# Kernel optimization log

Hardware: AMD Instinct MI355X
Metric: run time of the kernel (lower is better)

## Reference

```python
import jax, jax.numpy as jnp
import numpy as np

B, D, E, K, H = 16384, 1024, 6, 2, 256  # tokens, d_in, n_experts, top-k, expert hidden
EPS = 0.1  # epsilon default from forward signature


def setup_inputs() -> dict:
    key = jax.random.key(0)
    ks = jax.random.split(key, 4)
    scaled = lambda k, shp, fan: (jax.random.normal(k, shp, jnp.float32) / np.float32(np.sqrt(fan)))
    return {
        "x": jax.random.normal(ks[0], (B, D), jnp.float32),
        "Wr": scaled(ks[1], (D, E), D),
        "br": jnp.zeros((E,), jnp.float32),
        "W1": scaled(ks[2], (E, D, H), D),
        "b1": jnp.zeros((E, H), jnp.float32),
        "W2": scaled(ks[3], (E, H, D), H),
        "b2": jnp.zeros((E, D), jnp.float32),
    }


def reference(x, Wr, br, W1, b1, W2, b2):
    logits = x @ Wr + br                              # [B,E]
    probs = jax.nn.softmax(logits, axis=-1)
    En = probs.shape[-1]
    probs = (1.0 - EPS) * probs + EPS / En            # epsilon-annealed mix
    wts, idx = jax.lax.top_k(probs, K)                # [B,K] each, descending
    load = probs.mean(axis=0)                         # [E]
    aux = (load * jnp.log(load * En + 1e-9)).sum() / np.float32(np.log(En + 1e-9))
    # Dense all-expert evaluation (exact math of per-token expert MLPs), then gather top-k.
    h = jax.nn.gelu(jnp.einsum('bd,edh->ebh', x, W1) + b1[:, None, :], approximate=False)  # [E,B,H]
    ex_out = jnp.einsum('ebh,ehd->ebd', h, W2) + b2[:, None, :]                            # [E,B,D]
    tok = jnp.arange(x.shape[0])
    picked = ex_out[idx.T, tok[None, :]]              # [K,B,D] gather chosen experts
    out = jnp.einsum('bk,kbd->bd', wts, picked)       # weighted combine
    return out, aux
```

## Files before the change

### kernel.cpp

```cpp
#include <hip/hip_runtime.h>
#include <hip/hip_bf16.h>
#include <math.h>

#define B_TOK 16384
#define DDIM  1024
#define NEXP  6
#define NPAIR 15
#define HDIM  256
#define EPSF  0.1f
#define TILE  32
#define MAXTILES (B_TOK / TILE + NPAIR)

typedef float f32x4 __attribute__((ext_vector_type(4)));
typedef short bf16x8 __attribute__((ext_vector_type(8)));

__device__ __forceinline__ unsigned short f2bf(float f) {
    unsigned int u = __float_as_uint(f);
    u += 0x7FFFu + ((u >> 16) & 1u);
    return (unsigned short)(u >> 16);
}
__device__ __forceinline__ int pack2bf(float a, float b) {
    return (int)f2bf(a) | ((int)f2bf(b) << 16);
}
__device__ __forceinline__ float gelu_exact(float v) {
    return 0.5f * v * (1.0f + erff(v * 0.70710678118654752440f));
}

__global__ __launch_bounds__(256) void pack_w1_kernel(
    const float* __restrict__ W1, unsigned short* __restrict__ w1p) {
    const int lane = threadIdx.x & 63;
    const int blob = blockIdx.x * 4 + (threadIdx.x >> 6);
    const int e  = blob >> 9;
    const int rm = blob & 511;
    const int mg = rm >> 5;
    const int ks = rm & 31;
    const int d0 = ks * 32 + (lane >> 4) * 8;
    const int h  = mg * 16 + (lane & 15);
    const float* src = W1 + ((size_t)e * DDIM + d0) * HDIM + h;
    ushort4 o0, o1;
    o0.x = f2bf(src[0 * HDIM]); o0.y = f2bf(src[1 * HDIM]);
    o0.z = f2bf(src[2 * HDIM]); o0.w = f2bf(src[3 * HDIM]);
    o1.x = f2bf(src[4 * HDIM]); o1.y = f2bf(src[5 * HDIM]);
    o1.z = f2bf(src[6 * HDIM]); o1.w = f2bf(src[7 * HDIM]);
    unsigned short* dst = w1p + ((size_t)blob * 512) + lane * 8;
    *reinterpret_cast<ushort4*>(dst)     = o0;
    *reinterpret_cast<ushort4*>(dst + 4) = o1;
}

__global__ __launch_bounds__(256) void pack_w2_kernel(
    const float* __restrict__ W2, unsigned short* __restrict__ w2p) {
    const int lane = threadIdx.x & 63;
    const int blob = blockIdx.x * 4 + (threadIdx.x >> 6);
    const int e  = blob >> 9;
    const int rm = blob & 511;
    const int dg = rm >> 3;
    const int hs = rm & 7;
    const int h0 = hs * 32 + (lane >> 4) * 8;
    const int d  = dg * 16 + (lane & 15);
    const float* src = W2 + ((size_t)e * HDIM + h0) * DDIM + d;
    ushort4 o0, o1;
    o0.x = f2bf(src[0 * DDIM]); o0.y = f2bf(src[1 * DDIM]);
    o0.z = f2bf(src[2 * DDIM]); o0.w = f2bf(src[3 * DDIM]);
    o1.x = f2bf(src[4 * DDIM]); o1.y = f2bf(src[5 * DDIM]);
    o1.z = f2bf(src[6 * DDIM]); o1.w = f2bf(src[7 * DDIM]);
    unsigned short* dst = w2p + ((size_t)blob * 512) + lane * 8;
    *reinterpret_cast<ushort4*>(dst)     = o0;
    *reinterpret_cast<ushort4*>(dst + 4) = o1;
}

__global__ __launch_bounds__(256) void router1_kernel(
    const float* __restrict__ x, const float* __restrict__ Wr, const float* __restrict__ br,
    int* __restrict__ erec, float2* __restrict__ wrec, float* __restrict__ partial) {
    __shared__ float ls[NEXP];
    const int tid = threadIdx.x;
    if (tid < NEXP) ls[tid] = 0.0f;
    __syncthreads();

    const int wave = tid >> 6;
    const int lane = tid & 63;
    const int tok0 = blockIdx.x * 16 + wave * 4;

    float acc[4][NEXP];
#pragma unroll
    for (int j = 0; j < 4; ++j)
#pragma unroll
        for (int e = 0; e < NEXP; ++e) acc[j][e] = 0.0f;

#pragma unroll
    for (int it = 0; it < 4; ++it) {
        const float4* w4 = reinterpret_cast<const float4*>(
            Wr + (size_t)(it * 256 + lane * 4) * NEXP);
        float w[24];
#pragma unroll
        for (int q = 0; q < 6; ++q) *reinterpret_cast<float4*>(&w[q * 4]) = w4[q];
#pragma unroll
        for (int j = 0; j < 4; ++j) {
            float4 xv = reinterpret_cast<const float4*>(
                x + (size_t)(tok0 + j) * DDIM)[it * 64 + lane];
            float xa[4] = {xv.x, xv.y, xv.z, xv.w};
#pragma unroll
            for (int i2 = 0; i2 < 4; ++i2)
#pragma unroll
                for (int e = 0; e < NEXP; ++e)
                    acc[j][e] += xa[i2] * w[i2 * NEXP + e];
        }
    }

    float lsacc[NEXP];
#pragma unroll
    for (int e = 0; e < NEXP; ++e) lsacc[e] = 0.0f;

#pragma unroll
    for (int j = 0; j < 4; ++j) {
        float p[NEXP];
        float m = -1e30f;
#pragma unroll
        for (int e = 0; e < NEXP; ++e) {
            float v = acc[j][e];
#pragma unroll
            for (int off = 32; off > 0; off >>= 1) v += __shfl_xor(v, off, 64);
            p[e] = v + br[e];
            m = fmaxf(m, p[e]);
        }
        float s = 0.0f;
#pragma unroll
        for (int e = 0; e < NEXP; ++e) { p[e] = expf(p[e] - m); s += p[e]; }
        const float inv = (1.0f - EPSF) / s;
#pragma unroll
        for (int e = 0; e < NEXP; ++e) p[e] = p[e] * inv + EPSF / (float)NEXP;

        int b1i = 0; float bp = p[0];
#pragma unroll
        for (int e = 1; e < NEXP; ++e) if (p[e] > bp) { bp = p[e]; b1i = e; }
        int b2i = -1; float sp = -1e30f;
#pragma unroll
        for (int e = 0; e < NEXP; ++e) if (e != b1i && p[e] > sp) { sp = p[e]; b2i = e; }

        if (lane == 0) {
            erec[tok0 + j] = b1i | (b2i << 16);
            wrec[tok0 + j] = make_float2(bp, sp);
        }
#pragma unroll
        for (int e = 0; e < NEXP; ++e) lsacc[e] += p[e];
    }

    if (lane == 0) {
#pragma unroll
        for (int e = 0; e < NEXP; ++e) atomicAdd(&ls[e], lsacc[e]);
    }
    __syncthreads();
    if (tid < NEXP) partial[blockIdx.x * NEXP + tid] = ls[tid];
}

__global__ __launch_bounds__(1024) void router2_kernel(
    const int* __restrict__ erec, const float2* __restrict__ wrec,
    int* __restrict__ plist, float2* __restrict__ wpair, int* __restrict__ cnt) {
    __shared__ int lc[NPAIR];
    __shared__ int gb[NPAIR];
    const int tid = threadIdx.x;
    if (tid < NPAIR) lc[tid] = 0;
    __syncthreads();

    const int tok = blockIdx.x * 1024 + tid;
    const int er = erec[tok];
    const float2 wr = wrec[tok];
    const int e1 = er & 0xffff;
    const int e2 = er >> 16;
    const int a = min(e1, e2);
    const int b = max(e1, e2);
    const float wa = (a == e1) ? wr.x : wr.y;
    const float wb = (a == e1) ? wr.y : wr.x;
    const int p = a * (11 - a) / 2 + (b - a - 1);

    const int i = atomicAdd(&lc[p], 1);
    __syncthreads();
    if (tid < NPAIR) gb[tid] = atomicAdd(&cnt[tid], lc[tid]);
    __syncthreads();

    const int pos = gb[p] + i;
    plist[p * B_TOK + pos] = tok;
    wpair[p * B_TOK + pos] = make_float2(wa, wb);
}

__global__ void router3_aux_kernel(const int* __restrict__ cnt, int* __restrict__ table,
                                   const float* __restrict__ partial, float* __restrict__ out) {
    const int lane = threadIdx.x;
    if (lane == 0) {
        int off = 0;
        for (int p = 0; p < NPAIR; ++p) {
            const int t = (cnt[p] + TILE - 1) / TILE;
            for (int i = 0; i < t; ++i) table[1 + off + i] = (p << 16) | i;
            off += t;
        }
        table[0] = off;
    }
    float s[NEXP];
#pragma unroll
    for (int e = 0; e < NEXP; ++e) s[e] = 0.0f;
    for (int i = lane; i < 1024; i += 64) {
#pragma unroll
        for (int e = 0; e < NEXP; ++e) s[e] += partial[i * NEXP + e];
    }
#pragma unroll
    for (int e = 0; e < NEXP; ++e) {
        float v = s[e];
#pragma unroll
        for (int off = 32; off > 0; off >>= 1) v += __shfl_xor(v, off, 64);
        s[e] = v;
    }
    if (lane == 0) {
        float a = 0.0f;
#pragma unroll
        for (int e = 0; e < NEXP; ++e) {
            float ld = s[e] / (float)B_TOK;
            a += ld * logf(ld * (float)NEXP + 1e-9f);
        }
        out[(size_t)B_TOK * DDIM] = a / logf((float)NEXP + 1e-9f);
    }
}

__global__ __launch_bounds__(512, 2) void expert_kernel(
    const float* __restrict__ x,
    const unsigned short* __restrict__ w1p,
    const unsigned short* __restrict__ w2p,
    const float* __restrict__ b1,
    const float* __restrict__ b2,
    const int* __restrict__ plist, const float2* __restrict__ wpair,
    const int* __restrict__ cnt, const int* __restrict__ table,
    float* __restrict__ out) {
    const int g = blockIdx.x;
    if (g >= table[0]) return;
    const int code = table[1 + g];
    const int p = code >> 16;
    const int lt = code & 0xffff;
    const int n = cnt[p];

    int a, b;
    if      (p < 5)  { a = 0; b = p + 1; }
    else if (p < 9)  { a = 1; b = p - 3; }
    else if (p < 12) { a = 2; b = p - 6; }
    else if (p < 14) { a = 3; b = p - 8; }
    else             { a = 4; b = 5; }

    __shared__ int   tok_l[TILE];
    __shared__ float wa_l[TILE];
    __shared__ float wb_l[TILE];
    __shared__ __align__(16) char smem[65536];

    const int tid = threadIdx.x;
    const int lane = tid & 63;
    const int wave = tid >> 6;

    if (tid < TILE) {
        const int gi = lt * TILE + tid;
        if (gi < n) {
            tok_l[tid] = plist[p * B_TOK + gi];
            float2 w2v = wpair[p * B_TOK + gi];
            wa_l[tid] = w2v.x; wb_l[tid] = w2v.y;
        } else { tok_l[tid] = -1; wa_l[tid] = 0.0f; wb_l[tid] = 0.0f; }
    }
    __syncthreads();

    {
        const int ti = tid >> 4;
        const int q  = tid & 15;
        const int tok_s = tok_l[ti];
        const float* xrow = x + (size_t)(tok_s < 0 ? 0 : tok_s) * DDIM;
#pragma unroll
        for (int it = 0; it < 8; ++it) {
            const int k0 = it * 128 + q * 8;
            float4 f0, f1;
            if (tok_s >= 0) {
                const float4* ps = reinterpret_cast<const float4*>(xrow + k0);
                f0 = ps[0]; f1 = ps[1];
            } else {
                f0 = make_float4(0.f, 0.f, 0.f, 0.f); f1 = f0;
            }
            int4 wv;
            wv.x = pack2bf(f0.x, f0.y); wv.y = pack2bf(f0.z, f0.w);
            wv.z = pack2bf(f1.x, f1.y); wv.w = pack2bf(f1.z, f1.w);
            const int c = k0 >> 3;
            *reinterpret_cast<int4*>(smem + ti * 2048 + ((c ^ (ti & 7)) << 4)) = wv;
        }
    }
    __syncthreads();

    const int wexp = (wave < 4) ? a : b;
    const int hrow0 = (wave & 3) * 64;
    const int kofs = (lane >> 4) * 8;

    const unsigned short* w1base = w1p + ((size_t)wexp * 16 + (wave & 3) * 4) * 32 * 512
                                       + lane * 8;

    f32x4 zero4 = {0.f, 0.f, 0.f, 0.f};
    f32x4 acc[4][2];
#pragma unroll
    for (int i = 0; i < 4; ++i) { acc[i][0] = zero4; acc[i][1] = zero4; }

#pragma unroll 4
    for (int ks = 0; ks < 32; ++ks) {
        const int kk = ks * 32;
        bf16x8 aF[4], bF[2];
#pragma unroll
        for (int nt = 0; nt < 2; ++nt) {
            const int t = nt * 16 + (lane & 15);
            const int c = (kk >> 3) + (lane >> 4);
            bF[nt] = *reinterpret_cast<const bf16x8*>(
                smem + t * 2048 + ((c ^ (t & 7)) << 4));
        }
#pragma unroll
        for (int mt = 0; mt < 4; ++mt)
            aF[mt] = *reinterpret_cast<const bf16x8*>(
                w1base + ((size_t)mt * 32 + ks) * 512);
#pragma unroll
        for (int mt = 0; mt < 4; ++mt)
#pragma unroll
            for (int nt = 0; nt < 2; ++nt)
                acc[mt][nt] = __builtin_amdgcn_mfma_f32_16x16x32_bf16(
                    aF[mt], bF[nt], acc[mt][nt], 0, 0, 0);
    }
    __syncthreads();

    char* hdst = smem + ((wave < 4) ? 0 : 16384);
#pragma unroll
    for (int mt = 0; mt < 4; ++mt) {
        const int hh0 = hrow0 + mt * 16 + (lane >> 4) * 4;
        const float4 bb = *reinterpret_cast<const float4*>(b1 + wexp * HDIM + hh0);
#pragma unroll
        for (int nt = 0; nt < 2; ++nt) {
            const int t = nt * 16 + (lane & 15);
            const float wt = (wave < 4) ? wa_l[t] : wb_l[t];
            ushort4 hv;
            hv.x = f2bf(wt * gelu_exact(acc[mt][nt][0] + bb.x));
            hv.y = f2bf(wt * gelu_exact(acc[mt][nt][1] + bb.y));
            hv.z = f2bf(wt * gelu_exact(acc[mt][nt][2] + bb.z));
            hv.w = f2bf(wt * gelu_exact(acc[mt][nt][3] + bb.w));
            int off = t * 512 + hh0 * 2; off ^= (t & 7) << 4;
            *reinterpret_cast<ushort4*>(hdst + off) = hv;
        }
    }
    __syncthreads();

#pragma unroll 1
    for (int c2 = 0; c2 < 2; ++c2) {
        const int dbase = wave * 128 + c2 * 64;
        const unsigned short* w2abase = w2p + ((size_t)a * 64 + wave * 8 + c2 * 4) * 8 * 512
                                            + lane * 8;
        const unsigned short* w2bbase = w2p + ((size_t)b * 64 + wave * 8 + c2 * 4) * 8 * 512
                                            + lane * 8;
        f32x4 a2[2][4];
#pragma unroll
        for (int i = 0; i < 2; ++i)
#pragma unroll
            for (int j = 0; j < 4; ++j) a2[i][j] = zero4;

#pragma unroll
        for (int hs = 0; hs < 8; ++hs) {
            const int hh0 = hs * 32;
            bf16x8 aF[2], bF[4];
#pragma unroll
            for (int mt = 0; mt < 2; ++mt) {
                const int t = mt * 16 + (lane & 15);
                int off = t * 512 + (hh0 + kofs) * 2; off ^= (t & 7) << 4;
                aF[mt] = *reinterpret_cast<const bf16x8*>(smem + off);
            }
#pragma unroll
            for (int nt = 0; nt < 4; ++nt)
                bF[nt] = *reinterpret_cast<const bf16x8*>(
                    w2abase + ((size_t)nt * 8 + hs) * 512);
#pragma unroll
            for (int mt = 0; mt < 2; ++mt)
#pragma unroll
                for (int nt = 0; nt < 4; ++nt)
                    a2[mt][nt] = __builtin_amdgcn_mfma_f32_16x16x32_bf16(
                        aF[mt], bF[nt], a2[mt][nt], 0, 0, 0);
        }
#pragma unroll
        for (int hs = 0; hs < 8; ++hs) {
            const int hh0 = hs * 32;
            bf16x8 aF[2], bF[4];
#pragma unroll
            for (int mt = 0; mt < 2; ++mt) {
                const int t = mt * 16 + (lane & 15);
                int off = t * 512 + (hh0 + kofs) * 2; off ^= (t & 7) << 4;
                aF[mt] = *reinterpret_cast<const bf16x8*>(smem + 16384 + off);
            }
#pragma unroll
            for (int nt = 0; nt < 4; ++nt)
                bF[nt] = *reinterpret_cast<const bf16x8*>(
                    w2bbase + ((size_t)nt * 8 + hs) * 512);
#pragma unroll
            for (int mt = 0; mt < 2; ++mt)
#pragma unroll
                for (int nt = 0; nt < 4; ++nt)
                    a2[mt][nt] = __builtin_amdgcn_mfma_f32_16x16x32_bf16(
                        aF[mt], bF[nt], a2[mt][nt], 0, 0, 0);
        }

#pragma unroll
        for (int mt = 0; mt < 2; ++mt) {
            const int t0 = mt * 16 + (lane >> 4) * 4;
            int tkj[4]; float waj[4], wbj[4];
#pragma unroll
            for (int j = 0; j < 4; ++j) {
                tkj[j] = tok_l[t0 + j]; waj[j] = wa_l[t0 + j]; wbj[j] = wb_l[t0 + j];
            }
#pragma unroll
            for (int nt = 0; nt < 4; ++nt) {
                const int d = dbase + nt * 16 + (lane & 15);
                const float bA = b2[a * DDIM + d];
                const float bB = b2[b * DDIM + d];
#pragma unroll
                for (int j = 0; j < 4; ++j) {
                    if (tkj[j] >= 0)
                        out[(size_t)tkj[j] * DDIM + d] =
                            a2[mt][nt][j] + waj[j] * bA + wbj[j] * bB;
                }
            }
        }
    }
}

extern "C" void kernel_launch(void* const* d_in, const int* in_sizes, int n_in,
                              void* d_out, int out_size, void* d_ws, size_t ws_size,
                              hipStream_t stream) {
    const float* x  = (const float*)d_in[0];
    const float* Wr = (const float*)d_in[1];
    const float* br = (const float*)d_in[2];
    const float* W1 = (const float*)d_in[3];
    const float* b1 = (const float*)d_in[4];
    const float* W2 = (const float*)d_in[5];
    const float* b2 = (const float*)d_in[6];
    float* out = (float*)d_out;

    char* ws = (char*)d_ws;
    unsigned short* w1p   = (unsigned short*)(ws + 0);
    unsigned short* w2p   = (unsigned short*)(ws + 3145728);
    int*            plist = (int*)(ws + 6291456);
    float2*         wpair = (float2*)(ws + 7274496);
    int*            erec  = (int*)(ws + 9240576);
    float2*         wrec  = (float2*)(ws + 9306112);
    float*          partial = (float*)(ws + 9437184);
    int*            cnt   = (int*)(ws + 9461760);
    int*            table = (int*)(ws + 9462016);

    hipMemsetAsync(cnt, 0, 256, stream);

    pack_w1_kernel<<<dim3(768), dim3(256), 0, stream>>>(W1, w1p);
    pack_w2_kernel<<<dim3(768), dim3(256), 0, stream>>>(W2, w2p);

    router1_kernel<<<dim3(B_TOK / 16), dim3(256), 0, stream>>>(x, Wr, br, erec, wrec, partial);
    router2_kernel<<<dim3(B_TOK / 1024), dim3(1024), 0, stream>>>(erec, wrec, plist, wpair, cnt);
    router3_aux_kernel<<<1, 64, 0, stream>>>(cnt, table, partial, out);
    expert_kernel<<<dim3(MAXTILES), dim3(512), 0, stream>>>(
        x, w1p, w2p, b1, b2, plist, wpair, cnt, table, out);
}
```

Baseline: 302.3 us.

## Stream x tile through double-buffered LDS chunks to cut shared memory

The expert kernel no longer stages the full 32x1024 bf16 x tile in LDS before the first GEMM. It now loads x in eight 128-column chunks into a double buffer, prefetching the next chunk into registers while MFMAs run on the current one. This shrinks LDS use from 64KB to 48KB and raises launch bounds to 3 blocks per CU to improve occupancy. The cost is two extra barriers per chunk and more register pressure under the tighter occupancy bound.

```diff
diff --git a/kernel.cpp b/kernel.cpp
--- a/kernel.cpp
+++ b/kernel.cpp
@@ -219,7 +219,7 @@
     }
 }
 
-__global__ __launch_bounds__(512, 2) void expert_kernel(
+__global__ __launch_bounds__(512, 3) void expert_kernel(
     const float* __restrict__ x,
     const unsigned short* __restrict__ w1p,
     const unsigned short* __restrict__ w2p,
@@ -245,7 +245,7 @@
     __shared__ int   tok_l[TILE];
     __shared__ float wa_l[TILE];
     __shared__ float wb_l[TILE];
-    __shared__ __align__(16) char smem[65536];
+    __shared__ __align__(16) char smem[49152];
 
     const int tid = threadIdx.x;
     const int lane = tid & 63;
@@ -261,29 +261,11 @@
     }
     __syncthreads();
 
-    {
-        const int ti = tid >> 4;
-        const int q  = tid & 15;
-        const int tok_s = tok_l[ti];
-        const float* xrow = x + (size_t)(tok_s < 0 ? 0 : tok_s) * DDIM;
-#pragma unroll
-        for (int it = 0; it < 8; ++it) {
-            const int k0 = it * 128 + q * 8;
-            float4 f0, f1;
-            if (tok_s >= 0) {
-                const float4* ps = reinterpret_cast<const float4*>(xrow + k0);
-                f0 = ps[0]; f1 = ps[1];
-            } else {
-                f0 = make_float4(0.f, 0.f, 0.f, 0.f); f1 = f0;
-            }
-            int4 wv;
-            wv.x = pack2bf(f0.x, f0.y); wv.y = pack2bf(f0.z, f0.w);
-            wv.z = pack2bf(f1.x, f1.y); wv.w = pack2bf(f1.z, f1.w);
-            const int c = k0 >> 3;
-            *reinterpret_cast<int4*>(smem + ti * 2048 + ((c ^ (ti & 7)) << 4)) = wv;
-        }
-    }
-    __syncthreads();
+    const int ti = tid >> 4;
+    const int q  = tid & 15;
+    const int tok_s = tok_l[ti];
+    const float* xrow = x + (size_t)(tok_s < 0 ? 0 : tok_s) * DDIM;
+    const int woff = ti * 256 + ((q ^ (ti & 7)) << 4);
 
     const int wexp = (wave < 4) ? a : b;
     const int hrow0 = (wave & 3) * 64;
@@ -297,31 +279,59 @@
 #pragma unroll
     for (int i = 0; i < 4; ++i) { acc[i][0] = zero4; acc[i][1] = zero4; }
 
-#pragma unroll 4
-    for (int ks = 0; ks < 32; ++ks) {
-        const int kk = ks * 32;
-        bf16x8 aF[4], bF[2];
-#pragma unroll
-        for (int nt = 0; nt < 2; ++nt) {
-            const int t = nt * 16 + (lane & 15);
-            const int c = (kk >> 3) + (lane >> 4);
-            bF[nt] = *reinterpret_cast<const bf16x8*>(
-                smem + t * 2048 + ((c ^ (t & 7)) << 4));
-        }
-#pragma unroll
-        for (int mt = 0; mt < 4; ++mt)
-            aF[mt] = *reinterpret_cast<const bf16x8*>(
-                w1base + ((size_t)mt * 32 + ks) * 512);
-#pragma unroll
-        for (int mt = 0; mt < 4; ++mt)
-#pragma unroll
-            for (int nt = 0; nt < 2; ++nt)
-                acc[mt][nt] = __builtin_amdgcn_mfma_f32_16x16x32_bf16(
-                    aF[mt], bF[nt], acc[mt][nt], 0, 0, 0);
-    }
-    __syncthreads();
-
-    char* hdst = smem + ((wave < 4) ? 0 : 16384);
+    float4 pf0, pf1;
+    {
+        const float4* ps = reinterpret_cast<const float4*>(xrow + q * 8);
+        pf0 = ps[0]; pf1 = ps[1];
+        int4 wv;
+        wv.x = pack2bf(pf0.x, pf0.y); wv.y = pack2bf(pf0.z, pf0.w);
+        wv.z = pack2bf(pf1.x, pf1.y); wv.w = pack2bf(pf1.z, pf1.w);
+        if (tok_s < 0) wv = make_int4(0, 0, 0, 0);
+        *reinterpret_cast<int4*>(smem + woff) = wv;
+    }
+    __syncthreads();
+
+#pragma unroll 1
+    for (int c = 0; c < 8; ++c) {
+        char* cur = smem + ((c & 1) << 13);
+        char* nxt = smem + (((c + 1) & 1) << 13);
+        if (c < 7) {
+            const float4* ps = reinterpret_cast<const float4*>(xrow + (c + 1) * 128 + q * 8);
+            pf0 = ps[0]; pf1 = ps[1];
+        }
+#pragma unroll
+        for (int ks = 0; ks < 4; ++ks) {
+            bf16x8 aF[4], bF[2];
+#pragma unroll
+            for (int nt = 0; nt < 2; ++nt) {
+                const int t = nt * 16 + (lane & 15);
+                const int ci = ks * 4 + (lane >> 4);
+                bF[nt] = *reinterpret_cast<const bf16x8*>(
+                    cur + t * 256 + ((ci ^ (t & 7)) << 4));
+            }
+#pragma unroll
+            for (int mt = 0; mt < 4; ++mt)
+                aF[mt] = *reinterpret_cast<const bf16x8*>(
+                    w1base + ((size_t)mt * 32 + c * 4 + ks) * 512);
+#pragma unroll
+            for (int mt = 0; mt < 4; ++mt)
+#pragma unroll
+                for (int nt = 0; nt < 2; ++nt)
+                    acc[mt][nt] = __builtin_amdgcn_mfma_f32_16x16x32_bf16(
+                        aF[mt], bF[nt], acc[mt][nt], 0, 0, 0);
+        }
+        __syncthreads();
+        if (c < 7) {
+            int4 wv;
+            wv.x = pack2bf(pf0.x, pf0.y); wv.y = pack2bf(pf0.z, pf0.w);
+            wv.z = pack2bf(pf1.x, pf1.y); wv.w = pack2bf(pf1.z, pf1.w);
+            if (tok_s < 0) wv = make_int4(0, 0, 0, 0);
+            *reinterpret_cast<int4*>(nxt + woff) = wv;
+            __syncthreads();
+        }
+    }
+
+    char* hdst = smem + ((wave < 4) ? 16384 : 32768);
 #pragma unroll
     for (int mt = 0; mt < 4; ++mt) {
         const int hh0 = hrow0 + mt * 16 + (lane >> 4) * 4;
@@ -362,7 +372,7 @@
             for (int mt = 0; mt < 2; ++mt) {
                 const int t = mt * 16 + (lane & 15);
                 int off = t * 512 + (hh0 + kofs) * 2; off ^= (t & 7) << 4;
-                aF[mt] = *reinterpret_cast<const bf16x8*>(smem + off);
+                aF[mt] = *reinterpret_cast<const bf16x8*>(smem + 16384 + off);
             }
 #pragma unroll
             for (int nt = 0; nt < 4; ++nt)
@@ -383,7 +393,7 @@
             for (int mt = 0; mt < 2; ++mt) {
                 const int t = mt * 16 + (lane & 15);
                 int off = t * 512 + (hh0 + kofs) * 2; off ^= (t & 7) << 4;
-                aF[mt] = *reinterpret_cast<const bf16x8*>(smem + 16384 + off);
+                aF[mt] = *reinterpret_cast<const bf16x8*>(smem + 32768 + off);
             }
 #pragma unroll
             for (int nt = 0; nt < 4; ++nt)
```

Measured after the change: 373.3 us. +23.5%, slower.

## Interleave pair tiles across XCD-strided slots and use nontemporal x/out accesses

Applied to the files above, without the earlier changes.

The tile table is rebuilt as a fixed 768-slot array in which tiles of each expert pair are placed in slots congruent to pair mod 8. Blocks dispatched round-robin across the 8 XCDs therefore tend to keep the same expert weights in one XCD's L2. Empty slots hold -1 and those blocks exit early. Loads of x and stores of out now use nontemporal hints so they do not evict weights from cache. Costs are a serial placement loop on one thread, and a risk of overflow or idle blocks if tile counts exceed a residue class's capacity.

```diff
diff --git a/kernel.cpp b/kernel.cpp
--- a/kernel.cpp
+++ b/kernel.cpp
@@ -9,7 +9,7 @@
 #define HDIM  256
 #define EPSF  0.1f
 #define TILE  32
-#define MAXTILES (B_TOK / TILE + NPAIR)
+#define NSLOT 768
 
 typedef float f32x4 __attribute__((ext_vector_type(4)));
 typedef short bf16x8 __attribute__((ext_vector_type(8)));
@@ -182,40 +182,58 @@
     wpair[p * B_TOK + pos] = make_float2(wa, wb);
 }
 
-__global__ void router3_aux_kernel(const int* __restrict__ cnt, int* __restrict__ table,
-                                   const float* __restrict__ partial, float* __restrict__ out) {
-    const int lane = threadIdx.x;
-    if (lane == 0) {
-        int off = 0;
+__global__ __launch_bounds__(256) void router3_aux_kernel(
+    const int* __restrict__ cnt, int* __restrict__ table,
+    const float* __restrict__ partial, float* __restrict__ out) {
+    const int tid = threadIdx.x;
+    for (int i = tid; i < NSLOT; i += 256) table[i] = -1;
+    __syncthreads();
+
+    if (tid == 0) {
+        int jr[8] = {0, 0, 0, 0, 0, 0, 0, 0};
         for (int p = 0; p < NPAIR; ++p) {
             const int t = (cnt[p] + TILE - 1) / TILE;
-            for (int i = 0; i < t; ++i) table[1 + off + i] = (p << 16) | i;
-            off += t;
-        }
-        table[0] = off;
-    }
-    float s[NEXP];
-#pragma unroll
-    for (int e = 0; e < NEXP; ++e) s[e] = 0.0f;
-    for (int i = lane; i < 1024; i += 64) {
-#pragma unroll
-        for (int e = 0; e < NEXP; ++e) s[e] += partial[i * NEXP + e];
-    }
-#pragma unroll
-    for (int e = 0; e < NEXP; ++e) {
-        float v = s[e];
-#pragma unroll
-        for (int off = 32; off > 0; off >>= 1) v += __shfl_xor(v, off, 64);
-        s[e] = v;
-    }
-    if (lane == 0) {
-        float a = 0.0f;
+            const int r = p & 7;
+            for (int i = 0; i < t; ++i) {
+                int placed = -1;
+                while (jr[r] < NSLOT / 8) {
+                    const int s = r + 8 * jr[r];
+                    ++jr[r];
+                    if (table[s] < 0) { table[s] = (p << 16) | i; placed = s; break; }
+                }
+                if (placed < 0) {
+                    for (int s = 0; s < NSLOT; ++s)
+                        if (table[s] < 0) { table[s] = (p << 16) | i; break; }
+                }
+            }
+        }
+    }
+
+    if (tid < 64) {
+        const int lane = tid;
+        float s[NEXP];
+#pragma unroll
+        for (int e = 0; e < NEXP; ++e) s[e] = 0.0f;
+        for (int i = lane; i < 1024; i += 64) {
+#pragma unroll
+            for (int e = 0; e < NEXP; ++e) s[e] += partial[i * NEXP + e];
+        }
 #pragma unroll
         for (int e = 0; e < NEXP; ++e) {
-            float ld = s[e] / (float)B_TOK;
-            a += ld * logf(ld * (float)NEXP + 1e-9f);
-        }
-        out[(size_t)B_TOK * DDIM] = a / logf((float)NEXP + 1e-9f);
+            float v = s[e];
+#pragma unroll
+            for (int off = 32; off > 0; off >>= 1) v += __shfl_xor(v, off, 64);
+            s[e] = v;
+        }
+        if (lane == 0) {
+            float a = 0.0f;
+#pragma unroll
+            for (int e = 0; e < NEXP; ++e) {
+                float ld = s[e] / (float)B_TOK;
+                a += ld * logf(ld * (float)NEXP + 1e-9f);
+            }
+            out[(size_t)B_TOK * DDIM] = a / logf((float)NEXP + 1e-9f);
+        }
     }
 }
 
@@ -228,9 +246,8 @@
     const int* __restrict__ plist, const float2* __restrict__ wpair,
     const int* __restrict__ cnt, const int* __restrict__ table,
     float* __restrict__ out) {
-    const int g = blockIdx.x;
-    if (g >= table[0]) return;
-    const int code = table[1 + g];
+    const int code = table[blockIdx.x];
+    if (code < 0) return;
     const int p = code >> 16;
     const int lt = code & 0xffff;
     const int n = cnt[p];
@@ -269,12 +286,13 @@
 #pragma unroll
         for (int it = 0; it < 8; ++it) {
             const int k0 = it * 128 + q * 8;
-            float4 f0, f1;
+            f32x4 f0, f1;
             if (tok_s >= 0) {
-                const float4* ps = reinterpret_cast<const float4*>(xrow + k0);
-                f0 = ps[0]; f1 = ps[1];
+                const f32x4* ps = reinterpret_cast<const f32x4*>(xrow + k0);
+                f0 = __builtin_nontemporal_load(ps);
+                f1 = __builtin_nontemporal_load(ps + 1);
             } else {
-                f0 = make_float4(0.f, 0.f, 0.f, 0.f); f1 = f0;
+                f0 = (f32x4){0.f, 0.f, 0.f, 0.f}; f1 = f0;
             }
             int4 wv;
             wv.x = pack2bf(f0.x, f0.y); wv.y = pack2bf(f0.z, f0.w);
@@ -413,8 +431,9 @@
 #pragma unroll
                 for (int j = 0; j < 4; ++j) {
                     if (tkj[j] >= 0)
-                        out[(size_t)tkj[j] * DDIM + d] =
-                            a2[mt][nt][j] + waj[j] * bA + wbj[j] * bB;
+                        __builtin_nontemporal_store(
+                            a2[mt][nt][j] + waj[j] * bA + wbj[j] * bB,
+                            out + (size_t)tkj[j] * DDIM + d);
                 }
             }
         }
@@ -451,7 +470,7 @@
 
     router1_kernel<<<dim3(B_TOK / 16), dim3(256), 0, stream>>>(x, Wr, br, erec, wrec, partial);
     router2_kernel<<<dim3(B_TOK / 1024), dim3(1024), 0, stream>>>(erec, wrec, plist, wpair, cnt);
-    router3_aux_kernel<<<1, 64, 0, stream>>>(cnt, table, partial, out);
-    expert_kernel<<<dim3(MAXTILES), dim3(512), 0, stream>>>(
+    router3_aux_kernel<<<1, 256, 0, stream>>>(cnt, table, partial, out);
+    expert_kernel<<<dim3(NSLOT), dim3(512), 0, stream>>>(
         x, w1p, w2p, b1, b2, plist, wpair, cnt, table, out);
 }
```

Result: slower. 413.9 us (+36.9%).
